# Kernel tuning notes

Hardware: AMD Instinct MI355X
Metric: run time of the kernel (lower is better)

## Reference

```python
import jax, jax.numpy as jnp
import numpy as np

SQ, B, H, D = 2048, 1, 16, 64
HIDDEN = H * D


def setup_inputs() -> dict:
    key = jax.random.key(0)
    kq, kk, kv = jax.random.split(key, 3)
    query_layer = jax.random.normal(kq, (SQ, B, H, D), dtype=jnp.float32)
    key_layer = jax.random.normal(kk, (SQ, B, H, D), dtype=jnp.float32)
    value_layer = jax.random.normal(kv, (SQ, B, H, D), dtype=jnp.float32)
    return {"query_layer": query_layer, "key_layer": key_layer, "value_layer": value_layer}


def reference(query_layer, key_layer, value_layer):
    sq, b, h, d = query_layer.shape
    sk = key_layer.shape[0]
    norm = 1.0 / jnp.sqrt(jnp.asarray(d, dtype=query_layer.dtype))
    # scores: [b, h, sq, sk]  (materialized in the original via baddbmm)
    scores = jnp.einsum('sbhd,tbhd->bhst', query_layer, key_layer) * norm
    # causal mask (tril over [sq, sk]); masked positions -> -10000.0 as in original
    causal = jnp.tril(jnp.ones((sq, sk), dtype=bool))
    scores = jnp.where(causal[None, None], scores, jnp.asarray(-10000.0, scores.dtype))
    probs = jax.nn.softmax(scores, axis=-1)
    # context: [sq, b, h, d] -> [sq, b, hidden]
    ctx = jnp.einsum('bhst,tbhd->sbhd', probs, value_layer)
    return ctx.reshape(sq, b, h * d)
```

## Files before the change

kernel.cpp:

```cpp
#include <hip/hip_runtime.h>

typedef __bf16 bf16_t;
typedef bf16_t bf16x4 __attribute__((ext_vector_type(4)));
typedef bf16_t bf16x8 __attribute__((ext_vector_type(8)));
typedef float f32x4 __attribute__((ext_vector_type(4)));
typedef float f32x16 __attribute__((ext_vector_type(16)));

namespace {
constexpr int kNH  = 16;
constexpr int kHD  = 64;
constexpr int kHID = kNH * kHD;
constexpr int kKP  = 72;
constexpr int oQ = 0;
constexpr int oK = 64 * kKP;
constexpr int kOmPitch = 68;
constexpr int kSmBytes = 71680;
}

__global__ __launch_bounds__(256, 2)
void fattn_kernel(const float* __restrict__ Qg, const float* __restrict__ Kg,
                  const float* __restrict__ Vg, float* __restrict__ Og) {
  __shared__ __align__(16) unsigned char smraw[kSmBytes];
  bf16_t* sm = (bf16_t*)smraw;

  const int bid  = blockIdx.x;
  const int head = bid & (kNH - 1);
  const int mblk = 31 - (bid >> 4);
  const int m0   = mblk * 64;
  const int mtk  = 2 * mblk + 1;

  const int tid  = threadIdx.x;
  const int wave = tid >> 6;
  const int lane = tid & 63;
  const int h    = lane >> 5;
  const int m31  = lane & 31;

  bf16_t* qs = sm + oQ;
  bf16_t* ks = sm + oK + wave * 32 * kKP;

  const float kQScale = 0.125f * 1.44269504088896340736f;

  #pragma unroll
  for (int i = 0; i < 4; ++i) {
    const int idx = tid + 256 * i;
    const int row = idx >> 4;
    const int c4  = (idx & 15) * 4;
    const float4 f = *(const float4*)(Qg + (size_t)(m0 + row) * kHID + head * kHD + c4);
    bf16x4 hq;
    hq[0] = (bf16_t)(f.x * kQScale); hq[1] = (bf16_t)(f.y * kQScale);
    hq[2] = (bf16_t)(f.z * kQScale); hq[3] = (bf16_t)(f.w * kQScale);
    *(bf16x4*)(qs + row * kKP + c4) = hq;
  }
  __syncthreads();

  bf16x8 qf0[4], qf1[4];
  #pragma unroll
  for (int t = 0; t < 4; ++t) {
    qf0[t] = *(const bf16x8*)(qs + m31 * kKP + 16 * t + 8 * h);
    qf1[t] = *(const bf16x8*)(qs + (32 + m31) * kKP + 16 * t + 8 * h);
  }

  f32x16 Oa00, Oa10, Oa01, Oa11;
  #pragma unroll
  for (int r = 0; r < 16; ++r) { Oa00[r] = 0.f; Oa10[r] = 0.f; Oa01[r] = 0.f; Oa11[r] = 0.f; }
  float lacc0 = 0.f, lacc1 = 0.f;

  const int krow0 = lane >> 4;
  const int kc4   = (lane & 15) * 4;
  const float* kbase = Kg + head * kHD + kc4;
  const float* vbase = Vg + head * kHD + (size_t)(4 * h) * kHID + m31;

  float4 kreg[8];
  float  vv[32];

  if (wave <= mtk) {
    const int kv0 = wave * 32;
    #pragma unroll
    for (int i = 0; i < 8; ++i)
      kreg[i] = *(const float4*)(kbase + (size_t)(kv0 + krow0 + 4 * i) * kHID);
    const float* vt0 = vbase + (size_t)kv0 * kHID;
    #pragma unroll
    for (int db = 0; db < 2; ++db)
      #pragma unroll
      for (int tp = 0; tp < 2; ++tp)
        #pragma unroll
        for (int j = 0; j < 8; ++j)
          vv[db * 16 + tp * 8 + j] =
              vt0[(size_t)(16 * tp + (j & 3) + 8 * (j >> 2)) * kHID + 32 * db];
  }

  for (int jt = wave; jt <= mtk; jt += 4) {
    const int kv0 = jt * 32;

    #pragma unroll
    for (int i = 0; i < 8; ++i) {
      bf16x4 hk;
      hk[0] = (bf16_t)kreg[i].x; hk[1] = (bf16_t)kreg[i].y;
      hk[2] = (bf16_t)kreg[i].z; hk[3] = (bf16_t)kreg[i].w;
      *(bf16x4*)(ks + (krow0 + 4 * i) * kKP + kc4) = hk;
    }

    bf16x8 va0, va1, va2, va3;
    #pragma unroll
    for (int j = 0; j < 8; ++j) {
      va0[j] = (bf16_t)vv[j];
      va1[j] = (bf16_t)vv[8 + j];
      va2[j] = (bf16_t)vv[16 + j];
      va3[j] = (bf16_t)vv[24 + j];
    }

    if (jt + 4 <= mtk) {
      const int kn = (jt + 4) * 32;
      #pragma unroll
      for (int i = 0; i < 8; ++i)
        kreg[i] = *(const float4*)(kbase + (size_t)(kn + krow0 + 4 * i) * kHID);
      const float* vt0 = vbase + (size_t)kn * kHID;
      #pragma unroll
      for (int db = 0; db < 2; ++db)
        #pragma unroll
        for (int tp = 0; tp < 2; ++tp)
          #pragma unroll
          for (int j = 0; j < 8; ++j)
            vv[db * 16 + tp * 8 + j] =
                vt0[(size_t)(16 * tp + (j & 3) + 8 * (j >> 2)) * kHID + 32 * db];
    }

    f32x16 cs0, cs1;
    #pragma unroll
    for (int r = 0; r < 16; ++r) { cs0[r] = 0.f; cs1[r] = 0.f; }
    #pragma unroll
    for (int t = 0; t < 4; ++t) {
      bf16x8 af = *(const bf16x8*)(ks + m31 * kKP + 16 * t + 8 * h);
      cs0 = __builtin_amdgcn_mfma_f32_32x32x16_bf16(af, qf0[t], cs0, 0, 0, 0);
      cs1 = __builtin_amdgcn_mfma_f32_32x32x16_bf16(af, qf1[t], cs1, 0, 0, 0);
    }

    float p0[16], p1[16];
    if (jt >= mtk - 1) {
      const int qg0 = m0 + m31;
      const int qg1 = m0 + 32 + m31;
      #pragma unroll
      for (int r = 0; r < 16; ++r) {
        const int kg = kv0 + (r & 3) + 8 * (r >> 2) + 4 * h;
        const float e0 = __builtin_amdgcn_exp2f(cs0[r]);
        const float e1 = __builtin_amdgcn_exp2f(cs1[r]);
        p0[r] = (kg <= qg0) ? e0 : 0.f;
        p1[r] = (kg <= qg1) ? e1 : 0.f;
        lacc0 += p0[r];
        lacc1 += p1[r];
      }
    } else {
      #pragma unroll
      for (int r = 0; r < 16; ++r) {
        p0[r] = __builtin_amdgcn_exp2f(cs0[r]);
        p1[r] = __builtin_amdgcn_exp2f(cs1[r]);
        lacc0 += p0[r];
        lacc1 += p1[r];
      }
    }

    bf16x8 pa0, pa1, pb0, pb1;
    #pragma unroll
    for (int j = 0; j < 8; ++j) {
      pa0[j] = (bf16_t)p0[j];  pa1[j] = (bf16_t)p0[8 + j];
      pb0[j] = (bf16_t)p1[j];  pb1[j] = (bf16_t)p1[8 + j];
    }
    Oa00 = __builtin_amdgcn_mfma_f32_32x32x16_bf16(va0, pa0, Oa00, 0, 0, 0);
    Oa10 = __builtin_amdgcn_mfma_f32_32x32x16_bf16(va2, pa0, Oa10, 0, 0, 0);
    Oa01 = __builtin_amdgcn_mfma_f32_32x32x16_bf16(va0, pb0, Oa01, 0, 0, 0);
    Oa11 = __builtin_amdgcn_mfma_f32_32x32x16_bf16(va2, pb0, Oa11, 0, 0, 0);
    Oa00 = __builtin_amdgcn_mfma_f32_32x32x16_bf16(va1, pa1, Oa00, 0, 0, 0);
    Oa10 = __builtin_amdgcn_mfma_f32_32x32x16_bf16(va3, pa1, Oa10, 0, 0, 0);
    Oa01 = __builtin_amdgcn_mfma_f32_32x32x16_bf16(va1, pb1, Oa01, 0, 0, 0);
    Oa11 = __builtin_amdgcn_mfma_f32_32x32x16_bf16(va3, pb1, Oa11, 0, 0, 0);
  }

  __syncthreads();
  float* fv   = (float*)smraw;
  float* Om   = fv + wave * 64 * kOmPitch;
  float* larr = fv + 4 * 64 * kOmPitch;

  #pragma unroll
  for (int qh = 0; qh < 2; ++qh) {
    #pragma unroll
    for (int db = 0; db < 2; ++db) {
      const f32x16& Oa = (db == 0) ? (qh == 0 ? Oa00 : Oa01)
                                   : (qh == 0 ? Oa10 : Oa11);
      #pragma unroll
      for (int q = 0; q < 4; ++q) {
        f32x4 v;
        v[0] = Oa[4 * q + 0]; v[1] = Oa[4 * q + 1];
        v[2] = Oa[4 * q + 2]; v[3] = Oa[4 * q + 3];
        *(f32x4*)(Om + (size_t)(32 * qh + m31) * kOmPitch + 32 * db + 8 * q + 4 * h) = v;
      }
    }
  }
  larr[wave * 128 + lane]      = lacc0;
  larr[wave * 128 + 64 + lane] = lacc1;
  __syncthreads();

  #pragma unroll
  for (int i = 0; i < 4; ++i) {
    const int idx = tid + 256 * i;
    const int row = idx >> 4;
    const int c4  = (idx & 15) * 4;
    const int qh  = row >> 5;
    const int qm  = row & 31;

    float l = 0.f;
    #pragma unroll
    for (int w = 0; w < 4; ++w)
      l += larr[w * 128 + 64 * qh + qm] + larr[w * 128 + 64 * qh + 32 + qm];
    const float inv = 1.f / l;

    f32x4 o;
    #pragma unroll
    for (int e = 0; e < 4; ++e) o[e] = 0.f;
    #pragma unroll
    for (int w = 0; w < 4; ++w) {
      const f32x4 a = *(const f32x4*)(fv + w * 64 * kOmPitch + (size_t)row * kOmPitch + c4);
      #pragma unroll
      for (int e = 0; e < 4; ++e) o[e] += a[e];
    }
    #pragma unroll
    for (int e = 0; e < 4; ++e) o[e] *= inv;

    *(f32x4*)(Og + (size_t)(m0 + row) * kHID + head * kHD + c4) = o;
  }
}

extern "C" void kernel_launch(void* const* d_in, const int* in_sizes, int n_in,
                              void* d_out, int out_size, void* d_ws, size_t ws_size,
                              hipStream_t stream) {
  (void)in_sizes; (void)n_in; (void)d_ws; (void)ws_size; (void)out_size;
  const float* Q = (const float*)d_in[0];
  const float* K = (const float*)d_in[1];
  const float* V = (const float*)d_in[2];
  float* O = (float*)d_out;
  dim3 grid(512);
  dim3 block(256);
  hipLaunchKernelGGL(fattn_kernel, grid, block, 0, stream, Q, K, V, O);
}
```

Measured before the change: 105.0 us.

## Halve LDS epilogue buffer, reload Q fragments from LDS, skip fully masked half-tiles

Q fragments are no longer held in registers and are re-read from LDS for each KV tile. The per-wave output reduction runs in two 32-row halves, which halves the shared-memory footprint. The first query half now skips the last KV tile, where it is fully masked, and diagonal masking compares local indices only. Together this lowers register and LDS pressure so more blocks or waves fit per CU, at the cost of extra LDS reads and an added barrier round in the epilogue.

```diff
diff --git a/kernel.cpp b/kernel.cpp
--- a/kernel.cpp
+++ b/kernel.cpp
@@ -14,7 +14,7 @@
 constexpr int oQ = 0;
 constexpr int oK = 64 * kKP;
 constexpr int kOmPitch = 68;
-constexpr int kSmBytes = 71680;
+constexpr int kSmBytes = 35840;
 }
 
 __global__ __launch_bounds__(256, 2)
@@ -53,13 +53,6 @@
   }
   __syncthreads();
 
-  bf16x8 qf0[4], qf1[4];
-  #pragma unroll
-  for (int t = 0; t < 4; ++t) {
-    qf0[t] = *(const bf16x8*)(qs + m31 * kKP + 16 * t + 8 * h);
-    qf1[t] = *(const bf16x8*)(qs + (32 + m31) * kKP + 16 * t + 8 * h);
-  }
-
   f32x16 Oa00, Oa10, Oa01, Oa11;
   #pragma unroll
   for (int r = 0; r < 16; ++r) { Oa00[r] = 0.f; Oa10[r] = 0.f; Oa01[r] = 0.f; Oa11[r] = 0.f; }
@@ -125,107 +118,115 @@
                 vt0[(size_t)(16 * tp + (j & 3) + 8 * (j >> 2)) * kHID + 32 * db];
     }
 
-    f32x16 cs0, cs1;
-    #pragma unroll
-    for (int r = 0; r < 16; ++r) { cs0[r] = 0.f; cs1[r] = 0.f; }
-    #pragma unroll
-    for (int t = 0; t < 4; ++t) {
-      bf16x8 af = *(const bf16x8*)(ks + m31 * kKP + 16 * t + 8 * h);
-      cs0 = __builtin_amdgcn_mfma_f32_32x32x16_bf16(af, qf0[t], cs0, 0, 0, 0);
-      cs1 = __builtin_amdgcn_mfma_f32_32x32x16_bf16(af, qf1[t], cs1, 0, 0, 0);
-    }
-
-    float p0[16], p1[16];
-    if (jt >= mtk - 1) {
-      const int qg0 = m0 + m31;
-      const int qg1 = m0 + 32 + m31;
-      #pragma unroll
-      for (int r = 0; r < 16; ++r) {
-        const int kg = kv0 + (r & 3) + 8 * (r >> 2) + 4 * h;
-        const float e0 = __builtin_amdgcn_exp2f(cs0[r]);
-        const float e1 = __builtin_amdgcn_exp2f(cs1[r]);
-        p0[r] = (kg <= qg0) ? e0 : 0.f;
-        p1[r] = (kg <= qg1) ? e1 : 0.f;
-        lacc0 += p0[r];
-        lacc1 += p1[r];
-      }
-    } else {
-      #pragma unroll
-      for (int r = 0; r < 16; ++r) {
-        p0[r] = __builtin_amdgcn_exp2f(cs0[r]);
-        p1[r] = __builtin_amdgcn_exp2f(cs1[r]);
-        lacc0 += p0[r];
-        lacc1 += p1[r];
-      }
-    }
-
-    bf16x8 pa0, pa1, pb0, pb1;
-    #pragma unroll
-    for (int j = 0; j < 8; ++j) {
-      pa0[j] = (bf16_t)p0[j];  pa1[j] = (bf16_t)p0[8 + j];
-      pb0[j] = (bf16_t)p1[j];  pb1[j] = (bf16_t)p1[8 + j];
-    }
-    Oa00 = __builtin_amdgcn_mfma_f32_32x32x16_bf16(va0, pa0, Oa00, 0, 0, 0);
-    Oa10 = __builtin_amdgcn_mfma_f32_32x32x16_bf16(va2, pa0, Oa10, 0, 0, 0);
-    Oa01 = __builtin_amdgcn_mfma_f32_32x32x16_bf16(va0, pb0, Oa01, 0, 0, 0);
-    Oa11 = __builtin_amdgcn_mfma_f32_32x32x16_bf16(va2, pb0, Oa11, 0, 0, 0);
-    Oa00 = __builtin_amdgcn_mfma_f32_32x32x16_bf16(va1, pa1, Oa00, 0, 0, 0);
-    Oa10 = __builtin_amdgcn_mfma_f32_32x32x16_bf16(va3, pa1, Oa10, 0, 0, 0);
-    Oa01 = __builtin_amdgcn_mfma_f32_32x32x16_bf16(va1, pb1, Oa01, 0, 0, 0);
-    Oa11 = __builtin_amdgcn_mfma_f32_32x32x16_bf16(va3, pb1, Oa11, 0, 0, 0);
-  }
-
-  __syncthreads();
+    if (kv0 <= m0) {
+      f32x16 cs;
+      #pragma unroll
+      for (int r = 0; r < 16; ++r) cs[r] = 0.f;
+      #pragma unroll
+      for (int t = 0; t < 4; ++t) {
+        bf16x8 af = *(const bf16x8*)(ks + m31 * kKP + 16 * t + 8 * h);
+        bf16x8 qf = *(const bf16x8*)(qs + m31 * kKP + 16 * t + 8 * h);
+        cs = __builtin_amdgcn_mfma_f32_32x32x16_bf16(af, qf, cs, 0, 0, 0);
+      }
+      float p[16];
+      if (kv0 == m0) {
+        #pragma unroll
+        for (int r = 0; r < 16; ++r) {
+          const int kr = (r & 3) + 8 * (r >> 2) + 4 * h;
+          const float e = __builtin_amdgcn_exp2f(cs[r]);
+          p[r] = (kr <= m31) ? e : 0.f;
+          lacc0 += p[r];
+        }
+      } else {
+        #pragma unroll
+        for (int r = 0; r < 16; ++r) { p[r] = __builtin_amdgcn_exp2f(cs[r]); lacc0 += p[r]; }
+      }
+      bf16x8 pb0, pb1;
+      #pragma unroll
+      for (int j = 0; j < 8; ++j) { pb0[j] = (bf16_t)p[j]; pb1[j] = (bf16_t)p[8 + j]; }
+      Oa00 = __builtin_amdgcn_mfma_f32_32x32x16_bf16(va0, pb0, Oa00, 0, 0, 0);
+      Oa10 = __builtin_amdgcn_mfma_f32_32x32x16_bf16(va2, pb0, Oa10, 0, 0, 0);
+      Oa00 = __builtin_amdgcn_mfma_f32_32x32x16_bf16(va1, pb1, Oa00, 0, 0, 0);
+      Oa10 = __builtin_amdgcn_mfma_f32_32x32x16_bf16(va3, pb1, Oa10, 0, 0, 0);
+    }
+
+    {
+      f32x16 cs;
+      #pragma unroll
+      for (int r = 0; r < 16; ++r) cs[r] = 0.f;
+      #pragma unroll
+      for (int t = 0; t < 4; ++t) {
+        bf16x8 af = *(const bf16x8*)(ks + m31 * kKP + 16 * t + 8 * h);
+        bf16x8 qf = *(const bf16x8*)(qs + (32 + m31) * kKP + 16 * t + 8 * h);
+        cs = __builtin_amdgcn_mfma_f32_32x32x16_bf16(af, qf, cs, 0, 0, 0);
+      }
+      float p[16];
+      if (kv0 == m0 + 32) {
+        #pragma unroll
+        for (int r = 0; r < 16; ++r) {
+          const int kr = (r & 3) + 8 * (r >> 2) + 4 * h;
+          const float e = __builtin_amdgcn_exp2f(cs[r]);
+          p[r] = (kr <= m31) ? e : 0.f;
+          lacc1 += p[r];
+        }
+      } else {
+        #pragma unroll
+        for (int r = 0; r < 16; ++r) { p[r] = __builtin_amdgcn_exp2f(cs[r]); lacc1 += p[r]; }
+      }
+      bf16x8 pb0, pb1;
+      #pragma unroll
+      for (int j = 0; j < 8; ++j) { pb0[j] = (bf16_t)p[j]; pb1[j] = (bf16_t)p[8 + j]; }
+      Oa01 = __builtin_amdgcn_mfma_f32_32x32x16_bf16(va0, pb0, Oa01, 0, 0, 0);
+      Oa11 = __builtin_amdgcn_mfma_f32_32x32x16_bf16(va2, pb0, Oa11, 0, 0, 0);
+      Oa01 = __builtin_amdgcn_mfma_f32_32x32x16_bf16(va1, pb1, Oa01, 0, 0, 0);
+      Oa11 = __builtin_amdgcn_mfma_f32_32x32x16_bf16(va3, pb1, Oa11, 0, 0, 0);
+    }
+  }
+
   float* fv   = (float*)smraw;
-  float* Om   = fv + wave * 64 * kOmPitch;
-  float* larr = fv + 4 * 64 * kOmPitch;
+  float* Om   = fv + wave * 32 * kOmPitch;
+  float* larr = fv + 4 * 32 * kOmPitch;
 
   #pragma unroll
   for (int qh = 0; qh < 2; ++qh) {
-    #pragma unroll
-    for (int db = 0; db < 2; ++db) {
-      const f32x16& Oa = (db == 0) ? (qh == 0 ? Oa00 : Oa01)
-                                   : (qh == 0 ? Oa10 : Oa11);
+    __syncthreads();
+    {
+      const f32x16& A0 = qh ? Oa01 : Oa00;
+      const f32x16& A1 = qh ? Oa11 : Oa10;
       #pragma unroll
       for (int q = 0; q < 4; ++q) {
-        f32x4 v;
-        v[0] = Oa[4 * q + 0]; v[1] = Oa[4 * q + 1];
-        v[2] = Oa[4 * q + 2]; v[3] = Oa[4 * q + 3];
-        *(f32x4*)(Om + (size_t)(32 * qh + m31) * kOmPitch + 32 * db + 8 * q + 4 * h) = v;
-      }
-    }
-  }
-  larr[wave * 128 + lane]      = lacc0;
-  larr[wave * 128 + 64 + lane] = lacc1;
-  __syncthreads();
-
-  #pragma unroll
-  for (int i = 0; i < 4; ++i) {
-    const int idx = tid + 256 * i;
-    const int row = idx >> 4;
-    const int c4  = (idx & 15) * 4;
-    const int qh  = row >> 5;
-    const int qm  = row & 31;
-
-    float l = 0.f;
-    #pragma unroll
-    for (int w = 0; w < 4; ++w)
-      l += larr[w * 128 + 64 * qh + qm] + larr[w * 128 + 64 * qh + 32 + qm];
-    const float inv = 1.f / l;
-
-    f32x4 o;
-    #pragma unroll
-    for (int e = 0; e < 4; ++e) o[e] = 0.f;
-    #pragma unroll
-    for (int w = 0; w < 4; ++w) {
-      const f32x4 a = *(const f32x4*)(fv + w * 64 * kOmPitch + (size_t)row * kOmPitch + c4);
-      #pragma unroll
-      for (int e = 0; e < 4; ++e) o[e] += a[e];
-    }
-    #pragma unroll
-    for (int e = 0; e < 4; ++e) o[e] *= inv;
-
-    *(f32x4*)(Og + (size_t)(m0 + row) * kHID + head * kHD + c4) = o;
+        f32x4 v0, v1;
+        #pragma unroll
+        for (int e = 0; e < 4; ++e) { v0[e] = A0[4 * q + e]; v1[e] = A1[4 * q + e]; }
+        *(f32x4*)(Om + (size_t)m31 * kOmPitch + 8 * q + 4 * h)      = v0;
+        *(f32x4*)(Om + (size_t)m31 * kOmPitch + 32 + 8 * q + 4 * h) = v1;
+      }
+      larr[wave * 64 + lane] = qh ? lacc1 : lacc0;
+    }
+    __syncthreads();
+    #pragma unroll
+    for (int i = 0; i < 2; ++i) {
+      const int idx = tid + 256 * i;
+      const int row = idx >> 4;
+      const int c4  = (idx & 15) * 4;
+      float l = 0.f;
+      #pragma unroll
+      for (int w = 0; w < 4; ++w)
+        l += larr[w * 64 + row] + larr[w * 64 + 32 + row];
+      const float inv = 1.f / l;
+      f32x4 o;
+      #pragma unroll
+      for (int e = 0; e < 4; ++e) o[e] = 0.f;
+      #pragma unroll
+      for (int w = 0; w < 4; ++w) {
+        const f32x4 a = *(const f32x4*)(fv + w * 32 * kOmPitch + (size_t)row * kOmPitch + c4);
+        #pragma unroll
+        for (int e = 0; e < 4; ++e) o[e] += a[e];
+      }
+      #pragma unroll
+      for (int e = 0; e < 4; ++e) o[e] *= inv;
+      *(f32x4*)(Og + (size_t)(m0 + 32 * qh + row) * kHID + head * kHD + c4) = o;
+    }
   }
 }
 
```

After: 94.66 us. 1.11x faster.
